# Kernel tuning notes

Measured on AMD Instinct MI355X. Metric: run time of the kernel, lower is better.

## Reference

```python
import jax, jax.numpy as jnp
import numpy as np

N_EMBD = 384
HEAD_SIZE = 64
BLOCK_SIZE = 256

def setup_inputs() -> dict:
    key = jax.random.key(0)
    kx, kk, kq, kv = jax.random.split(key, 4)
    bound = 1.0 / np.sqrt(N_EMBD)  # torch nn.Linear default init
    return {
        "x": jax.random.normal(kx, (512, 256, N_EMBD), dtype=jnp.float32),
        "Wk": jax.random.uniform(kk, (N_EMBD, HEAD_SIZE), jnp.float32, -bound, bound),
        "Wq": jax.random.uniform(kq, (N_EMBD, HEAD_SIZE), jnp.float32, -bound, bound),
        "Wv": jax.random.uniform(kv, (N_EMBD, HEAD_SIZE), jnp.float32, -bound, bound),
    }

def reference(x, Wk, Wq, Wv):
    # x: [B, T, C]; single causal self-attention head (eval mode: dropout off)
    B, T, C = x.shape
    k = jnp.einsum('btc,ch->bth', x, Wk)   # [B, T, H]
    q = jnp.einsum('btc,ch->bth', x, Wq)
    v = jnp.einsum('btc,ch->bth', x, Wv)
    scale = 1.0 / jnp.sqrt(jnp.asarray(k.shape[-1], dtype=x.dtype))
    wei = jnp.einsum('bth,bsh->bts', q, k) * scale  # [B, T, T]
    causal = jnp.tril(jnp.ones((T, T), dtype=bool))
    wei = jnp.where(causal, wei, -jnp.inf)
    wei = jax.nn.softmax(wei, axis=-1)
    return jnp.einsum('bts,bsh->bth', wei, v)  # [B, T, H]
```

## Files before the change

kernel.cpp:

```cpp
#include <hip/hip_runtime.h>

#define T_DIM 256
#define C_DIM 384
#define H_DIM 64

typedef __attribute__((ext_vector_type(4))) float f32x4;
typedef __attribute__((ext_vector_type(8))) short bf16x8;
typedef unsigned short u16;

__device__ __forceinline__ u16 f2b(float f) {
  unsigned u = __float_as_uint(f);
  u = (u + 0x7FFFu + ((u >> 16) & 1u)) >> 16;
  return (u16)u;
}
__device__ __forceinline__ unsigned pkbf(float a, float b) {
  unsigned r;
  asm("v_cvt_pk_bf16_f32 %0, %1, %2" : "=v"(r) : "v"(a), "v"(b));
  return r;
}

__device__ __forceinline__ int sw64(int r, int c)  { return r * 64  + (c ^ ((r & 7) << 3)); }
__device__ __forceinline__ int sw256(int h, int t) { return h * 256 + (t ^ ((h & 7) << 3)); }
__device__ __forceinline__ int sw32(int r, int c)  { return r * 32  + (c ^ (((r >> 1) & 3) << 3)); }

__global__ __launch_bounds__(512, 2)
void head_fused(const float* __restrict__ x,
                const float* __restrict__ Wk,
                const float* __restrict__ Wq,
                const float* __restrict__ Wv,
                float* __restrict__ out)
{
  __shared__ u16 sh[32768];
  u16* xs  = sh;
  u16* wsT = sh + 8192;
  u16* ks  = sh;
  u16* vT  = sh + 16384;

  const int tid  = threadIdx.x;
  const int wv   = tid >> 6;
  const int lane = tid & 63;
  const int g    = lane >> 4;
  const int lr   = lane & 15;
  const int b    = blockIdx.x;

  const float* xb = x + (size_t)b * (T_DIM * C_DIM);

  int xr[4], xc[4];
#pragma unroll
  for (int it = 0; it < 4; ++it) {
    int idx = tid + it * 512;
    xr[it] = idx >> 3;
    xc[it] = (idx & 7) * 4;
  }
  int wrow[3], wcc[3];
  const float* wsrc[3];
#pragma unroll
  for (int it = 0; it < 3; ++it) {
    int idx = tid + it * 512;
    int q   = idx >> 5;
    int cc  = idx & 31;
    int seg = q >> 4;
    int hq  = q & 15;
    wrow[it] = seg * 64 + hq * 4;
    wcc[it]  = cc;
    wsrc[it] = ((seg == 0) ? Wq : (seg == 1) ? Wk : Wv) + hq * 4;
  }

  f32x4 acc[2][12];
#pragma unroll
  for (int mi = 0; mi < 2; ++mi)
#pragma unroll
    for (int nj = 0; nj < 12; ++nj)
      acc[mi][nj] = (f32x4){0.f, 0.f, 0.f, 0.f};

  f32x4 px[4], pwv[3];
#pragma unroll
  for (int it = 0; it < 4; ++it)
    px[it] = *reinterpret_cast<const f32x4*>(xb + xr[it] * C_DIM + xc[it]);
#pragma unroll
  for (int it = 0; it < 3; ++it)
    pwv[it] = *reinterpret_cast<const f32x4*>(wsrc[it] + wcc[it] * H_DIM);

  for (int kt = 0; kt < 12; ++kt) {
    __syncthreads();
#pragma unroll
    for (int it = 0; it < 4; ++it) {
      uint2 pv;
      pv.x = (unsigned)f2b(px[it][0]) | ((unsigned)f2b(px[it][1]) << 16);
      pv.y = (unsigned)f2b(px[it][2]) | ((unsigned)f2b(px[it][3]) << 16);
      *reinterpret_cast<uint2*>(&xs[sw32(xr[it], xc[it])]) = pv;
    }
#pragma unroll
    for (int it = 0; it < 3; ++it) {
      wsT[sw32(wrow[it] + 0, wcc[it])] = f2b(pwv[it][0]);
      wsT[sw32(wrow[it] + 1, wcc[it])] = f2b(pwv[it][1]);
      wsT[sw32(wrow[it] + 2, wcc[it])] = f2b(pwv[it][2]);
      wsT[sw32(wrow[it] + 3, wcc[it])] = f2b(pwv[it][3]);
    }
    if (kt < 11) {
      int kk = (kt + 1) * 32;
#pragma unroll
      for (int it = 0; it < 4; ++it)
        px[it] = *reinterpret_cast<const f32x4*>(xb + xr[it] * C_DIM + kk + xc[it]);
#pragma unroll
      for (int it = 0; it < 3; ++it)
        pwv[it] = *reinterpret_cast<const f32x4*>(wsrc[it] + (kk + wcc[it]) * H_DIM);
    }
    __syncthreads();

    bf16x8 afr[2];
#pragma unroll
    for (int mi = 0; mi < 2; ++mi)
      afr[mi] = *reinterpret_cast<const bf16x8*>(&xs[sw32(wv * 32 + mi * 16 + lr, g * 8)]);
#pragma unroll
    for (int nj = 0; nj < 12; ++nj) {
      bf16x8 bfr = *reinterpret_cast<const bf16x8*>(&wsT[sw32(nj * 16 + lr, g * 8)]);
#pragma unroll
      for (int mi = 0; mi < 2; ++mi)
        acc[mi][nj] = __builtin_amdgcn_mfma_f32_16x16x32_bf16(afr[mi], bfr, acc[mi][nj], 0, 0, 0);
    }
  }

  __syncthreads();

  u16* slab = sh + wv * 2048;
#pragma unroll
  for (int mi = 0; mi < 2; ++mi)
#pragma unroll
    for (int nj = 0; nj < 4; ++nj)
#pragma unroll
      for (int e = 0; e < 4; ++e)
        slab[sw64(mi * 16 + g * 4 + e, nj * 16 + lr)] = f2b(acc[mi][nj][e]);
  asm volatile("s_waitcnt lgkmcnt(0)" ::: "memory");

  bf16x8 qf[2][2];
#pragma unroll
  for (int mi = 0; mi < 2; ++mi)
#pragma unroll
    for (int kb = 0; kb < 2; ++kb)
      qf[mi][kb] = *reinterpret_cast<const bf16x8*>(&slab[sw64(mi * 16 + lr, kb * 32 + g * 8)]);
  __syncthreads();

#pragma unroll
  for (int mi = 0; mi < 2; ++mi)
#pragma unroll
    for (int nj = 4; nj < 12; ++nj)
#pragma unroll
      for (int e = 0; e < 4; ++e) {
        int r = wv * 32 + mi * 16 + g * 4 + e;
        int n = nj * 16 + lr;
        u16 val = f2b(acc[mi][nj][e]);
        if (n < 128) ks[sw64(r, n - 64)] = val;
        else         vT[sw256(n - 128, r)] = val;
      }
  __syncthreads();

  const int r0   = wv * 32;
  const int jmax = wv >> 1;

  f32x4 o[2][4];
  float m_run[2], l_run[2];
#pragma unroll
  for (int mi = 0; mi < 2; ++mi) {
    m_run[mi] = -__builtin_inff();
    l_run[mi] = 0.f;
#pragma unroll
    for (int nh = 0; nh < 4; ++nh) o[mi][nh] = (f32x4){0.f, 0.f, 0.f, 0.f};
  }

  for (int j = 0; j <= jmax; ++j) {
    f32x4 sT[2][4];
#pragma unroll
    for (int mi = 0; mi < 2; ++mi)
#pragma unroll
      for (int ni = 0; ni < 4; ++ni)
        sT[mi][ni] = (f32x4){0.f, 0.f, 0.f, 0.f};
#pragma unroll
    for (int kb = 0; kb < 2; ++kb) {
#pragma unroll
      for (int ni = 0; ni < 4; ++ni) {
        bf16x8 kf = *reinterpret_cast<const bf16x8*>(&ks[sw64(j * 64 + ni * 16 + lr, kb * 32 + g * 8)]);
#pragma unroll
        for (int mi = 0; mi < 2; ++mi)
          sT[mi][ni] = __builtin_amdgcn_mfma_f32_16x16x32_bf16(kf, qf[mi][kb], sT[mi][ni], 0, 0, 0);
      }
    }

#pragma unroll
    for (int mi = 0; mi < 2; ++mi) {
      const int q = r0 + mi * 16 + lr;
      float pm = -__builtin_inff();
#pragma unroll
      for (int ni = 0; ni < 4; ++ni)
#pragma unroll
        for (int e = 0; e < 4; ++e) {
          float v = sT[mi][ni][e] * 0.125f;
          int kv = j * 64 + ni * 16 + g * 4 + e;
          v = (kv > q) ? -__builtin_inff() : v;
          sT[mi][ni][e] = v;
          pm = fmaxf(pm, v);
        }
      pm = fmaxf(pm, __shfl_xor(pm, 16));
      pm = fmaxf(pm, __shfl_xor(pm, 32));

      float mn = fmaxf(m_run[mi], pm);
      float alpha = __expf(m_run[mi] - mn);
      m_run[mi] = mn;
      float rs = 0.f;
#pragma unroll
      for (int ni = 0; ni < 4; ++ni)
#pragma unroll
        for (int e = 0; e < 4; ++e) {
          float p = __expf(sT[mi][ni][e] - mn);
          sT[mi][ni][e] = p;
          rs += p;
        }
      rs += __shfl_xor(rs, 16);
      rs += __shfl_xor(rs, 32);
      l_run[mi] = l_run[mi] * alpha + rs;

#pragma unroll
      for (int e = 0; e < 4; ++e) {
        float am = __shfl(alpha, g * 4 + e);
#pragma unroll
        for (int nh = 0; nh < 4; ++nh) o[mi][nh][e] *= am;
      }
    }

    union PA { unsigned w[4]; bf16x8 v; };
    PA pa[2][2];
#pragma unroll
    for (int mi = 0; mi < 2; ++mi) {
      unsigned pk[4][2];
#pragma unroll
      for (int ni = 0; ni < 4; ++ni) {
        pk[ni][0] = pkbf(sT[mi][ni][0], sT[mi][ni][1]);
        pk[ni][1] = pkbf(sT[mi][ni][2], sT[mi][ni][3]);
      }
#pragma unroll
      for (int kb = 0; kb < 2; ++kb)
#pragma unroll
        for (int w = 0; w < 4; ++w) {
          int sl = ((2 * g + (w >> 1)) & 3) * 16 + lr;
          unsigned lo = __shfl(pk[2 * kb + 0][w & 1], sl);
          unsigned hi = __shfl(pk[2 * kb + 1][w & 1], sl);
          pa[mi][kb].w[w] = (g >= 2) ? hi : lo;
        }
    }

#pragma unroll
    for (int kb = 0; kb < 2; ++kb) {
#pragma unroll
      for (int nh = 0; nh < 4; ++nh) {
        bf16x8 vf = *reinterpret_cast<const bf16x8*>(&vT[sw256(nh * 16 + lr, j * 64 + kb * 32 + g * 8)]);
#pragma unroll
        for (int mi = 0; mi < 2; ++mi)
          o[mi][nh] = __builtin_amdgcn_mfma_f32_16x16x32_bf16(pa[mi][kb].v, vf, o[mi][nh], 0, 0, 0);
      }
    }
  }

  float* ob = out + (size_t)b * (T_DIM * H_DIM);
#pragma unroll
  for (int mi = 0; mi < 2; ++mi) {
    float linv[4];
#pragma unroll
    for (int e = 0; e < 4; ++e)
      linv[e] = 1.f / __shfl(l_run[mi], g * 4 + e);
#pragma unroll
    for (int nh = 0; nh < 4; ++nh)
#pragma unroll
      for (int e = 0; e < 4; ++e) {
        int r = r0 + mi * 16 + g * 4 + e;
        int h = nh * 16 + lr;
        ob[r * H_DIM + h] = o[mi][nh][e] * linv[e];
      }
  }
}

extern "C" void kernel_launch(void* const* d_in, const int* in_sizes, int n_in,
                              void* d_out, int out_size, void* d_ws, size_t ws_size,
                              hipStream_t stream) {
  const float* x  = (const float*)d_in[0];
  const float* Wk = (const float*)d_in[1];
  const float* Wq = (const float*)d_in[2];
  const float* Wv = (const float*)d_in[3];
  float* out = (float*)d_out;
  int B = in_sizes[0] / (T_DIM * C_DIM);
  head_fused<<<dim3(B), dim3(512), 0, stream>>>(x, Wk, Wq, Wv, out);
}
```

Baseline: 62.76 us.

## Pretranspose weights to bf16 and read B fragments from global, drop block barriers

A small prologue kernel converts Wq/Wk/Wv to a transposed bf16 buffer in the workspace, so the main kernel loads MFMA B fragments straight from global/L2 instead of staging weights through LDS every k-step. Each wave now stages only its own 32 rows of x into double-buffered LDS, which removes the two __syncthreads per k-tile in favour of a local lgkmcnt wait. This trades barrier and LDS-write costs for extra global loads of weight fragments per wave and an extra kernel launch.

```diff
diff --git a/kernel.cpp b/kernel.cpp
--- a/kernel.cpp
+++ b/kernel.cpp
@@ -23,16 +23,25 @@
 __device__ __forceinline__ int sw256(int h, int t) { return h * 256 + (t ^ ((h & 7) << 3)); }
 __device__ __forceinline__ int sw32(int r, int c)  { return r * 32  + (c ^ (((r >> 1) & 3) << 3)); }
 
+__global__ void wtrans_k(const float* __restrict__ Wq, const float* __restrict__ Wk,
+                         const float* __restrict__ Wv, u16* __restrict__ wt)
+{
+  int blk = blockIdx.x;
+  int seg = blk / 96;
+  int id  = (blk % 96) * 256 + threadIdx.x;
+  int h = id & 63, k = id >> 6;
+  const float* W = (seg == 0) ? Wq : (seg == 1) ? Wk : Wv;
+  wt[(seg * 64 + h) * C_DIM + k] = f2b(W[k * H_DIM + h]);
+}
+
 __global__ __launch_bounds__(512, 2)
 void head_fused(const float* __restrict__ x,
-                const float* __restrict__ Wk,
-                const float* __restrict__ Wq,
-                const float* __restrict__ Wv,
+                const u16*   __restrict__ wt,
                 float* __restrict__ out)
 {
   __shared__ u16 sh[32768];
-  u16* xs  = sh;
-  u16* wsT = sh + 8192;
+  u16* xsA = sh;
+  u16* xsB = sh + 8192;
   u16* ks  = sh;
   u16* vT  = sh + 16384;
 
@@ -45,26 +54,11 @@
 
   const float* xb = x + (size_t)b * (T_DIM * C_DIM);
 
-  int xr[4], xc[4];
-#pragma unroll
-  for (int it = 0; it < 4; ++it) {
-    int idx = tid + it * 512;
-    xr[it] = idx >> 3;
-    xc[it] = (idx & 7) * 4;
-  }
-  int wrow[3], wcc[3];
-  const float* wsrc[3];
-#pragma unroll
-  for (int it = 0; it < 3; ++it) {
-    int idx = tid + it * 512;
-    int q   = idx >> 5;
-    int cc  = idx & 31;
-    int seg = q >> 4;
-    int hq  = q & 15;
-    wrow[it] = seg * 64 + hq * 4;
-    wcc[it]  = cc;
-    wsrc[it] = ((seg == 0) ? Wq : (seg == 1) ? Wk : Wv) + hq * 4;
-  }
+  const int srow = wv * 32 + (lane & 31);
+  const int scg  = (lane >> 5) * 16;
+  const float* xsrc = xb + srow * C_DIM + scg;
+
+  const u16* wb = wt + (size_t)lr * C_DIM + g * 8;
 
   f32x4 acc[2][12];
 #pragma unroll
@@ -73,40 +67,27 @@
     for (int nj = 0; nj < 12; ++nj)
       acc[mi][nj] = (f32x4){0.f, 0.f, 0.f, 0.f};
 
-  f32x4 px[4], pwv[3];
-#pragma unroll
-  for (int it = 0; it < 4; ++it)
-    px[it] = *reinterpret_cast<const f32x4*>(xb + xr[it] * C_DIM + xc[it]);
-#pragma unroll
-  for (int it = 0; it < 3; ++it)
-    pwv[it] = *reinterpret_cast<const f32x4*>(wsrc[it] + wcc[it] * H_DIM);
+  f32x4 px[4];
+#pragma unroll
+  for (int i = 0; i < 4; ++i)
+    px[i] = *reinterpret_cast<const f32x4*>(xsrc + i * 4);
 
   for (int kt = 0; kt < 12; ++kt) {
-    __syncthreads();
-#pragma unroll
-    for (int it = 0; it < 4; ++it) {
-      uint2 pv;
-      pv.x = (unsigned)f2b(px[it][0]) | ((unsigned)f2b(px[it][1]) << 16);
-      pv.y = (unsigned)f2b(px[it][2]) | ((unsigned)f2b(px[it][3]) << 16);
-      *reinterpret_cast<uint2*>(&xs[sw32(xr[it], xc[it])]) = pv;
-    }
-#pragma unroll
-    for (int it = 0; it < 3; ++it) {
-      wsT[sw32(wrow[it] + 0, wcc[it])] = f2b(pwv[it][0]);
-      wsT[sw32(wrow[it] + 1, wcc[it])] = f2b(pwv[it][1]);
-      wsT[sw32(wrow[it] + 2, wcc[it])] = f2b(pwv[it][2]);
-      wsT[sw32(wrow[it] + 3, wcc[it])] = f2b(pwv[it][3]);
-    }
+    u16* xs = (kt & 1) ? xsB : xsA;
+    uint4 w0, w1;
+    w0.x = pkbf(px[0][0], px[0][1]);  w0.y = pkbf(px[0][2], px[0][3]);
+    w0.z = pkbf(px[1][0], px[1][1]);  w0.w = pkbf(px[1][2], px[1][3]);
+    w1.x = pkbf(px[2][0], px[2][1]);  w1.y = pkbf(px[2][2], px[2][3]);
+    w1.z = pkbf(px[3][0], px[3][1]);  w1.w = pkbf(px[3][2], px[3][3]);
+    *reinterpret_cast<uint4*>(&xs[sw32(srow, scg)])     = w0;
+    *reinterpret_cast<uint4*>(&xs[sw32(srow, scg + 8)]) = w1;
     if (kt < 11) {
-      int kk = (kt + 1) * 32;
-#pragma unroll
-      for (int it = 0; it < 4; ++it)
-        px[it] = *reinterpret_cast<const f32x4*>(xb + xr[it] * C_DIM + kk + xc[it]);
-#pragma unroll
-      for (int it = 0; it < 3; ++it)
-        pwv[it] = *reinterpret_cast<const f32x4*>(wsrc[it] + (kk + wcc[it]) * H_DIM);
-    }
-    __syncthreads();
+      const float* p = xsrc + (kt + 1) * 32;
+#pragma unroll
+      for (int i = 0; i < 4; ++i)
+        px[i] = *reinterpret_cast<const f32x4*>(p + i * 4);
+    }
+    asm volatile("s_waitcnt lgkmcnt(0)" ::: "memory");
 
     bf16x8 afr[2];
 #pragma unroll
@@ -114,10 +95,9 @@
       afr[mi] = *reinterpret_cast<const bf16x8*>(&xs[sw32(wv * 32 + mi * 16 + lr, g * 8)]);
 #pragma unroll
     for (int nj = 0; nj < 12; ++nj) {
-      bf16x8 bfr = *reinterpret_cast<const bf16x8*>(&wsT[sw32(nj * 16 + lr, g * 8)]);
-#pragma unroll
-      for (int mi = 0; mi < 2; ++mi)
-        acc[mi][nj] = __builtin_amdgcn_mfma_f32_16x16x32_bf16(afr[mi], bfr, acc[mi][nj], 0, 0, 0);
+      bf16x8 bfr = *reinterpret_cast<const bf16x8*>(wb + nj * (16 * C_DIM) + kt * 32);
+      acc[0][nj] = __builtin_amdgcn_mfma_f32_16x16x32_bf16(afr[0], bfr, acc[0][nj], 0, 0, 0);
+      acc[1][nj] = __builtin_amdgcn_mfma_f32_16x16x32_bf16(afr[1], bfr, acc[1][nj], 0, 0, 0);
     }
   }
 
@@ -286,6 +266,9 @@
   const float* Wq = (const float*)d_in[2];
   const float* Wv = (const float*)d_in[3];
   float* out = (float*)d_out;
+  u16* wt = (u16*)d_ws;
   int B = in_sizes[0] / (T_DIM * C_DIM);
-  head_fused<<<dim3(B), dim3(512), 0, stream>>>(x, Wk, Wq, Wv, out);
-}
+
+  wtrans_k<<<dim3(288), dim3(256), 0, stream>>>(Wq, Wk, Wv, wt);
+  head_fused<<<dim3(B), dim3(512), 0, stream>>>(x, wt, out);
+}
```

New measurement: 116.4 us. 85.4% more time.
